# Kernel tuning notes

Measured on AMD Instinct MI355X. Metric: run time of the kernel, lower is better.

Reference implementation:

```python
import jax, jax.numpy as jnp
import numpy as np

D_MODEL = 1024
N_HEADS = 16
D_HEAD = D_MODEL // N_HEADS


def setup_inputs() -> dict:
    key = jax.random.key(0)
    k1, k2, k3 = jax.random.split(key, 3)
    x = jax.random.normal(k1, (4, 2048, D_MODEL), dtype=jnp.float32)
    # nn.Linear weights stored [out, in]; we keep that convention.
    s = 1.0 / np.sqrt(D_MODEL)
    W_qkv = jax.random.uniform(k2, (3 * D_MODEL, D_MODEL), dtype=jnp.float32, minval=-s, maxval=s)
    W_out = jax.random.uniform(k3, (D_MODEL, D_MODEL), dtype=jnp.float32, minval=-s, maxval=s)
    return {"x": x, "W_qkv": W_qkv, "W_out": W_out}


def reference(x, W_qkv, W_out):
    B, T, C = x.shape
    qkv = jnp.einsum('btc,oc->bto', x, W_qkv)  # [B,T,3C]
    q, k, v = jnp.split(qkv, 3, axis=-1)

    def split_heads(t):
        return t.reshape(B, T, N_HEADS, D_HEAD).transpose(0, 2, 1, 3)  # [B,H,T,Dh]

    q, k, v = split_heads(q), split_heads(k), split_heads(v)
    scale = D_HEAD ** -0.5
    scores = jnp.einsum('bhqd,bhkd->bhqk', q, k) * scale  # [B,H,T,T]
    mask = jnp.triu(jnp.ones((T, T), dtype=bool), k=1)
    scores = jnp.where(mask, -jnp.inf, scores)
    att = jax.nn.softmax(scores, axis=-1)
    out = jnp.einsum('bhqk,bhkd->bhqd', att, v)
    out = out.transpose(0, 2, 1, 3).reshape(B, T, C)
    return jnp.einsum('btc,oc->bto', out, W_out)
```

## Files before the change

### kernel.cpp

```cpp
#include <hip/hip_runtime.h>
#include <hip/hip_bf16.h>
#include <math.h>


typedef __attribute__((ext_vector_type(8))) short bf16x8;
typedef __attribute__((ext_vector_type(4))) float f32x4;

__device__ __forceinline__ void async16(const void* g, void* l) {
    __builtin_amdgcn_global_load_lds((const __attribute__((address_space(1))) void*)g,
                                     (__attribute__((address_space(3))) void*)l,
                                     16, 0, 0);
}

__device__ __forceinline__ unsigned short f2b(float f) {
    __hip_bfloat16 h = __float2bfloat16(f);
    return *(unsigned short*)&h;
}

__global__ __launch_bounds__(256)
void cast_f32_bf16(const float* __restrict__ in, unsigned short* __restrict__ out, int n)
{
    int i = (blockIdx.x * 256 + threadIdx.x) * 8;
    if (i + 8 > n) return;
    float4 a = *(const float4*)(in + i);
    float4 b = *(const float4*)(in + i + 4);
    __hip_bfloat16 r[8];
    r[0] = __float2bfloat16(a.x); r[1] = __float2bfloat16(a.y);
    r[2] = __float2bfloat16(a.z); r[3] = __float2bfloat16(a.w);
    r[4] = __float2bfloat16(b.x); r[5] = __float2bfloat16(b.y);
    r[6] = __float2bfloat16(b.z); r[7] = __float2bfloat16(b.w);
    *(float4*)(out + i) = *(float4*)r;
}

template <typename OutT>
__global__ __launch_bounds__(256)
void gemm_bf16_nt(const unsigned short* __restrict__ A,
                  const unsigned short* __restrict__ Bt,
                  OutT* __restrict__ C, int M, int N, int K,
                  int sc_ncols, float sc)
{
    __shared__ unsigned short As[128 * 32];
    __shared__ unsigned short Bs[128 * 32];
    const int tid  = threadIdx.x;
    const int lane = tid & 63;
    const int wave = tid >> 6;
    const int wm   = wave >> 1;
    const int wn   = wave & 1;
    const int m0   = blockIdx.y * 128;
    const int n0   = blockIdx.x * 128;

    f32x4 acc[4][4];
#pragma unroll
    for (int i = 0; i < 4; ++i)
#pragma unroll
        for (int j = 0; j < 4; ++j) acc[i][j] = (f32x4){0.f, 0.f, 0.f, 0.f};

    const int srow = tid >> 2;
    const int scol = (tid & 3) * 8;
    const int wbase = wave * 512;
    const int fr = lane & 15;
    const int fk = (lane >> 4) * 8;

    for (int k0 = 0; k0 < K; k0 += 32) {
#pragma unroll
        for (int c = 0; c < 2; ++c) {
            const unsigned short* ga = A + (size_t)(m0 + c * 64 + srow) * K + k0 + scol;
            async16(ga, As + c * 2048 + wbase);
            const unsigned short* gb = Bt + (size_t)(n0 + c * 64 + srow) * K + k0 + scol;
            async16(gb, Bs + c * 2048 + wbase);
        }
        __syncthreads();

        bf16x8 af[4], bfr[4];
#pragma unroll
        for (int mi = 0; mi < 4; ++mi)
            af[mi] = *(const bf16x8*)&As[(wm * 64 + mi * 16 + fr) * 32 + fk];
#pragma unroll
        for (int ni = 0; ni < 4; ++ni)
            bfr[ni] = *(const bf16x8*)&Bs[(wn * 64 + ni * 16 + fr) * 32 + fk];
#pragma unroll
        for (int mi = 0; mi < 4; ++mi)
#pragma unroll
            for (int ni = 0; ni < 4; ++ni)
                acc[mi][ni] = __builtin_amdgcn_mfma_f32_16x16x32_bf16(
                    af[mi], bfr[ni], acc[mi][ni], 0, 0, 0);
        __syncthreads();
    }

    const int ccol  = n0 + wn * 64 + (lane & 15);
    const int crow0 = m0 + wm * 64 + (lane >> 4) * 4;
#pragma unroll
    for (int mi = 0; mi < 4; ++mi) {
#pragma unroll
        for (int r = 0; r < 4; ++r) {
            const size_t row = (size_t)(crow0 + mi * 16 + r);
#pragma unroll
            for (int ni = 0; ni < 4; ++ni) {
                float mult = (ccol + ni * 16 < sc_ncols) ? sc : 1.0f;
                float v = acc[mi][ni][r] * mult;
                if constexpr (__is_same(OutT, float)) {
                    C[row * N + ccol + ni * 16] = v;
                } else {
                    C[row * N + ccol + ni * 16] = f2b(v);
                }
            }
        }
    }
}

__global__ __launch_bounds__(256)
void transpose_v(const unsigned short* __restrict__ qkv, unsigned short* __restrict__ vt, int T)
{
    __shared__ unsigned short tile[64 * 72];
    const int tid = threadIdx.x;
    const int k0  = blockIdx.x * 64;
    const int h   = blockIdx.y;
    const int b   = blockIdx.z;
    const size_t C3 = 3072;
    const unsigned short* vb = qkv + (size_t)b * T * C3 + 2048 + h * 64;

    const int r  = tid >> 2;
    const int c0 = (tid & 3) * 16;
    {
        const unsigned short* g = vb + (size_t)(k0 + r) * C3 + c0;
        *(float4*)&tile[r * 72 + c0]     = *(const float4*)g;
        *(float4*)&tile[r * 72 + c0 + 8] = *(const float4*)(g + 8);
    }
    __syncthreads();
    unsigned short buf[16];
#pragma unroll
    for (int j = 0; j < 16; ++j) buf[j] = tile[(c0 + j) * 72 + r];
    unsigned short* o = vt + ((size_t)(b * 16 + h) * 64 + r) * T + k0 + c0;
    *(float4*)o       = *(float4*)&buf[0];
    *(float4*)(o + 8) = *(float4*)&buf[8];
}

__global__ __launch_bounds__(256, 4)
void attn_mfma(const unsigned short* __restrict__ qkv,
               const unsigned short* __restrict__ vt,
               unsigned short* __restrict__ out, int T)
{
    __shared__ unsigned short Ks[64 * 72];
    __shared__ unsigned short Vts[64 * 72];
    __shared__ unsigned short Ps[64 * 72];

    const int tid  = threadIdx.x;
    const int lane = tid & 63;
    const int wave = tid >> 6;
    const int lc   = lane & 15;
    const int quad = lane >> 4;
    const int nq   = T >> 6;
    const int bid  = blockIdx.x;
    const int bh   = bid & 63;
    const int a    = bid >> 6;
    const int b    = bh >> 4;
    const int h    = bh & 15;
    int qt[2];
    qt[0] = nq - 1 - a;
    qt[1] = a;
    const size_t C3 = 3072;
    const unsigned short* qb  = qkv + (size_t)b * T * C3 + h * 64;
    const unsigned short* kb  = qb + 1024;
    const unsigned short* vtb = vt + (size_t)(b * 16 + h) * 64 * T;

    const int sr = tid >> 2;
    const int sc = (tid & 3) * 16;

    const int qrow = wave * 16 + lc;
    bf16x8 qf[2][2];
#pragma unroll
    for (int t = 0; t < 2; ++t) {
        const unsigned short* gq = qb + (size_t)(qt[t] * 64 + qrow) * C3 + quad * 8;
        qf[t][0] = *(const bf16x8*)gq;
        qf[t][1] = *(const bf16x8*)(gq + 32);
    }

    f32x4 o_[2][4];
    float l_[2][4];
#pragma unroll
    for (int t = 0; t < 2; ++t)
#pragma unroll
        for (int i = 0; i < 4; ++i) {
            o_[t][i] = (f32x4){0.f, 0.f, 0.f, 0.f};
            l_[t][i] = 0.f;
        }

    const float MB = 8.0f;

    for (int kt = 0; kt <= qt[0]; ++kt) {
        const int k0 = kt * 64;
        const unsigned short* gk = kb + (size_t)(k0 + sr) * C3 + sc;
        float4 kv0 = *(const float4*)gk;
        float4 kv1 = *(const float4*)(gk + 8);
        const unsigned short* gv = vtb + (size_t)sr * T + k0 + sc;
        float4 vv0 = *(const float4*)gv;
        float4 vv1 = *(const float4*)(gv + 8);

        __syncthreads();
        *(float4*)&Ks[sr * 72 + sc]      = kv0;
        *(float4*)&Ks[sr * 72 + sc + 8]  = kv1;
        *(float4*)&Vts[sr * 72 + sc]     = vv0;
        *(float4*)&Vts[sr * 72 + sc + 8] = vv1;
        __syncthreads();

#pragma unroll
        for (int t = 0; t < 2; ++t) {
            if (t == 1 && kt > qt[1]) break;
            const bool isdiag = (kt == qt[t]);

            f32x4 s[4];
#pragma unroll
            for (int ni = 0; ni < 4; ++ni) {
                bf16x8 bk0 = *(const bf16x8*)&Ks[(ni * 16 + lc) * 72 + quad * 8];
                bf16x8 bk1 = *(const bf16x8*)&Ks[(ni * 16 + lc) * 72 + 32 + quad * 8];
                s[ni] = (f32x4){0.f, 0.f, 0.f, 0.f};
                s[ni] = __builtin_amdgcn_mfma_f32_16x16x32_bf16(qf[t][0], bk0, s[ni], 0, 0, 0);
                s[ni] = __builtin_amdgcn_mfma_f32_16x16x32_bf16(qf[t][1], bk1, s[ni], 0, 0, 0);
            }
            if (isdiag) {
#pragma unroll
                for (int ni = 0; ni < 4; ++ni)
#pragma unroll
                    for (int r = 0; r < 4; ++r)
                        if (ni * 16 + lc > wave * 16 + quad * 4 + r)
                            s[ni][r] = -__builtin_inff();
            }
#pragma unroll
            for (int r = 0; r < 4; ++r) {
                float p0 = __builtin_amdgcn_exp2f(s[0][r] - MB);
                float p1 = __builtin_amdgcn_exp2f(s[1][r] - MB);
                float p2 = __builtin_amdgcn_exp2f(s[2][r] - MB);
                float p3 = __builtin_amdgcn_exp2f(s[3][r] - MB);
                l_[t][r] += (p0 + p1) + (p2 + p3);
                const int prow = (wave * 16 + quad * 4 + r) * 72;
                Ps[prow + lc]      = f2b(p0);
                Ps[prow + 16 + lc] = f2b(p1);
                Ps[prow + 32 + lc] = f2b(p2);
                Ps[prow + 48 + lc] = f2b(p3);
            }
            bf16x8 ap0 = *(const bf16x8*)&Ps[(wave * 16 + lc) * 72 + quad * 8];
            bf16x8 ap1 = *(const bf16x8*)&Ps[(wave * 16 + lc) * 72 + 32 + quad * 8];
#pragma unroll
            for (int ni = 0; ni < 4; ++ni) {
                bf16x8 bv0 = *(const bf16x8*)&Vts[(ni * 16 + lc) * 72 + quad * 8];
                bf16x8 bv1 = *(const bf16x8*)&Vts[(ni * 16 + lc) * 72 + 32 + quad * 8];
                o_[t][ni] = __builtin_amdgcn_mfma_f32_16x16x32_bf16(ap0, bv0, o_[t][ni], 0, 0, 0);
                o_[t][ni] = __builtin_amdgcn_mfma_f32_16x16x32_bf16(ap1, bv1, o_[t][ni], 0, 0, 0);
            }
        }
    }

#pragma unroll
    for (int t = 0; t < 2; ++t) {
        unsigned short* ob = out + ((size_t)b * T + qt[t] * 64 + wave * 16 + quad * 4) * 1024
                           + h * 64 + lc;
#pragma unroll
        for (int r = 0; r < 4; ++r) {
            float rs = l_[t][r];
#pragma unroll
            for (int off = 1; off < 16; off <<= 1)
                rs += __shfl_xor(rs, off, 16);
            float inv = 1.f / rs;
#pragma unroll
            for (int ni = 0; ni < 4; ++ni)
                ob[(size_t)r * 1024 + ni * 16] = f2b(o_[t][ni][r] * inv);
        }
    }
}

extern "C" void kernel_launch(void* const* d_in, const int* in_sizes, int n_in,
                              void* d_out, int out_size, void* d_ws, size_t ws_size,
                              hipStream_t stream)
{
    const float* x     = (const float*)d_in[0];
    const float* W_qkv = (const float*)d_in[1];
    const float* W_out = (const float*)d_in[2];
    float* out = (float*)d_out;

    const int C = 1024;
    const int T = 2048;
    const int M = in_sizes[0] / C;
    const int B = M / T;
    const int n_x    = in_sizes[0];
    const int n_wqkv = in_sizes[1];
    const int n_wout = in_sizes[2];

    unsigned short* x_bf    = (unsigned short*)d_ws;
    unsigned short* wqkv_bf = x_bf    + n_x;
    unsigned short* wout_bf = wqkv_bf + n_wqkv;
    unsigned short* qkv_bf  = wout_bf + n_wout;
    unsigned short* vt_bf   = qkv_bf  + (size_t)M * 3 * C;
    unsigned short* ao_bf   = vt_bf   + (size_t)B * 16 * 64 * T;

    cast_f32_bf16<<<n_x    / 2048, 256, 0, stream>>>(x,     x_bf,    n_x);
    cast_f32_bf16<<<n_wqkv / 2048, 256, 0, stream>>>(W_qkv, wqkv_bf, n_wqkv);
    cast_f32_bf16<<<n_wout / 2048, 256, 0, stream>>>(W_out, wout_bf, n_wout);

    const float QSC = 0.18033688011112042f;
    gemm_bf16_nt<unsigned short><<<dim3((3*C)/128, M/128), 256, 0, stream>>>(
        x_bf, wqkv_bf, qkv_bf, M, 3*C, C, C, QSC);

    transpose_v<<<dim3(T/64, 16, B), 256, 0, stream>>>(qkv_bf, vt_bf, T);

    const int nq = T / 64;
    attn_mfma<<<dim3(B * 16 * (nq / 2)), 256, 0, stream>>>(qkv_bf, vt_bf, ao_bf, T);

    gemm_bf16_nt<float><<<dim3(C/128, M/128), 256, 0, stream>>>(
        ao_bf, wout_bf, out, M, C, C, 0, 1.0f);
}
```

Baseline: 272.9 us.

## Transpose attention MFMA operands so scores land per-query-row in lanes

Swaps MFMA operand order (K and V^T as A, Q and P as B) so each lane holds four consecutive key/feature values for one query row. This allows packed bf16x2 stores of P to LDS and of the output to global memory, and a per-lane row-sum reduced with two shuffles instead of four shuffle rounds per row. K and V fragments are hoisted out of the per-tile loop and shared by both query tiles, and P gets a double buffer so both tiles' softmax can run before either PV matmul. The cost is higher register pressure from the hoisted fragments under launch_bounds(256,4), plus extra LDS for the second P buffer.

```diff
diff --git a/kernel.cpp b/kernel.cpp
--- a/kernel.cpp
+++ b/kernel.cpp
@@ -15,6 +15,11 @@
 __device__ __forceinline__ unsigned short f2b(float f) {
     __hip_bfloat16 h = __float2bfloat16(f);
     return *(unsigned short*)&h;
+}
+
+__device__ __forceinline__ unsigned int packbf2(float a, float b) {
+    __hip_bfloat162 h2 = __float22bfloat162_rn(make_float2(a, b));
+    return *(unsigned int*)&h2;
 }
 
 __global__ __launch_bounds__(256)
@@ -142,7 +147,7 @@
 {
     __shared__ unsigned short Ks[64 * 72];
     __shared__ unsigned short Vts[64 * 72];
-    __shared__ unsigned short Ps[64 * 72];
+    __shared__ unsigned short Ps[2][64 * 72];
 
     const int tid  = threadIdx.x;
     const int lane = tid & 63;
@@ -176,14 +181,13 @@
     }
 
     f32x4 o_[2][4];
-    float l_[2][4];
-#pragma unroll
-    for (int t = 0; t < 2; ++t)
-#pragma unroll
-        for (int i = 0; i < 4; ++i) {
-            o_[t][i] = (f32x4){0.f, 0.f, 0.f, 0.f};
-            l_[t][i] = 0.f;
-        }
+    float l_[2];
+#pragma unroll
+    for (int t = 0; t < 2; ++t) {
+        l_[t] = 0.f;
+#pragma unroll
+        for (int i = 0; i < 4; ++i) o_[t][i] = (f32x4){0.f, 0.f, 0.f, 0.f};
+    }
 
     const float MB = 8.0f;
 
@@ -203,67 +207,84 @@
         *(float4*)&Vts[sr * 72 + sc + 8] = vv1;
         __syncthreads();
 
+        bf16x8 ak[4][2];
+#pragma unroll
+        for (int mi = 0; mi < 4; ++mi) {
+            ak[mi][0] = *(const bf16x8*)&Ks[(mi * 16 + lc) * 72 + quad * 8];
+            ak[mi][1] = *(const bf16x8*)&Ks[(mi * 16 + lc) * 72 + 32 + quad * 8];
+        }
+
 #pragma unroll
         for (int t = 0; t < 2; ++t) {
             if (t == 1 && kt > qt[1]) break;
-            const bool isdiag = (kt == qt[t]);
-
             f32x4 s[4];
 #pragma unroll
-            for (int ni = 0; ni < 4; ++ni) {
-                bf16x8 bk0 = *(const bf16x8*)&Ks[(ni * 16 + lc) * 72 + quad * 8];
-                bf16x8 bk1 = *(const bf16x8*)&Ks[(ni * 16 + lc) * 72 + 32 + quad * 8];
-                s[ni] = (f32x4){0.f, 0.f, 0.f, 0.f};
-                s[ni] = __builtin_amdgcn_mfma_f32_16x16x32_bf16(qf[t][0], bk0, s[ni], 0, 0, 0);
-                s[ni] = __builtin_amdgcn_mfma_f32_16x16x32_bf16(qf[t][1], bk1, s[ni], 0, 0, 0);
-            }
-            if (isdiag) {
-#pragma unroll
-                for (int ni = 0; ni < 4; ++ni)
+            for (int mi = 0; mi < 4; ++mi) {
+                s[mi] = (f32x4){0.f, 0.f, 0.f, 0.f};
+                s[mi] = __builtin_amdgcn_mfma_f32_16x16x32_bf16(ak[mi][0], qf[t][0], s[mi], 0, 0, 0);
+                s[mi] = __builtin_amdgcn_mfma_f32_16x16x32_bf16(ak[mi][1], qf[t][1], s[mi], 0, 0, 0);
+            }
+            if (kt == qt[t]) {
+                const int qg = qt[t] * 64 + wave * 16 + lc;
+                const int kbase = k0 + quad * 4;
+#pragma unroll
+                for (int mi = 0; mi < 4; ++mi)
 #pragma unroll
                     for (int r = 0; r < 4; ++r)
-                        if (ni * 16 + lc > wave * 16 + quad * 4 + r)
-                            s[ni][r] = -__builtin_inff();
-            }
-#pragma unroll
-            for (int r = 0; r < 4; ++r) {
-                float p0 = __builtin_amdgcn_exp2f(s[0][r] - MB);
-                float p1 = __builtin_amdgcn_exp2f(s[1][r] - MB);
-                float p2 = __builtin_amdgcn_exp2f(s[2][r] - MB);
-                float p3 = __builtin_amdgcn_exp2f(s[3][r] - MB);
-                l_[t][r] += (p0 + p1) + (p2 + p3);
-                const int prow = (wave * 16 + quad * 4 + r) * 72;
-                Ps[prow + lc]      = f2b(p0);
-                Ps[prow + 16 + lc] = f2b(p1);
-                Ps[prow + 32 + lc] = f2b(p2);
-                Ps[prow + 48 + lc] = f2b(p3);
-            }
-            bf16x8 ap0 = *(const bf16x8*)&Ps[(wave * 16 + lc) * 72 + quad * 8];
-            bf16x8 ap1 = *(const bf16x8*)&Ps[(wave * 16 + lc) * 72 + 32 + quad * 8];
-#pragma unroll
-            for (int ni = 0; ni < 4; ++ni) {
-                bf16x8 bv0 = *(const bf16x8*)&Vts[(ni * 16 + lc) * 72 + quad * 8];
-                bf16x8 bv1 = *(const bf16x8*)&Vts[(ni * 16 + lc) * 72 + 32 + quad * 8];
-                o_[t][ni] = __builtin_amdgcn_mfma_f32_16x16x32_bf16(ap0, bv0, o_[t][ni], 0, 0, 0);
-                o_[t][ni] = __builtin_amdgcn_mfma_f32_16x16x32_bf16(ap1, bv1, o_[t][ni], 0, 0, 0);
+                        if (kbase + mi * 16 + r > qg)
+                            s[mi][r] = -__builtin_inff();
+            }
+            float lacc = 0.f;
+            const int prow = (wave * 16 + lc) * 72 + quad * 4;
+#pragma unroll
+            for (int mi = 0; mi < 4; ++mi) {
+                float p0 = __builtin_amdgcn_exp2f(s[mi][0] - MB);
+                float p1 = __builtin_amdgcn_exp2f(s[mi][1] - MB);
+                float p2 = __builtin_amdgcn_exp2f(s[mi][2] - MB);
+                float p3 = __builtin_amdgcn_exp2f(s[mi][3] - MB);
+                lacc += (p0 + p1) + (p2 + p3);
+                uint2 pk;
+                pk.x = packbf2(p0, p1);
+                pk.y = packbf2(p2, p3);
+                *(uint2*)&Ps[t][prow + mi * 16] = pk;
+            }
+            l_[t] += lacc;
+        }
+
+        bf16x8 av[4][2];
+#pragma unroll
+        for (int mi = 0; mi < 4; ++mi) {
+            av[mi][0] = *(const bf16x8*)&Vts[(mi * 16 + lc) * 72 + quad * 8];
+            av[mi][1] = *(const bf16x8*)&Vts[(mi * 16 + lc) * 72 + 32 + quad * 8];
+        }
+
+#pragma unroll
+        for (int t = 0; t < 2; ++t) {
+            if (t == 1 && kt > qt[1]) break;
+            bf16x8 bp0 = *(const bf16x8*)&Ps[t][(wave * 16 + lc) * 72 + quad * 8];
+            bf16x8 bp1 = *(const bf16x8*)&Ps[t][(wave * 16 + lc) * 72 + 32 + quad * 8];
+#pragma unroll
+            for (int mi = 0; mi < 4; ++mi) {
+                o_[t][mi] = __builtin_amdgcn_mfma_f32_16x16x32_bf16(av[mi][0], bp0, o_[t][mi], 0, 0, 0);
+                o_[t][mi] = __builtin_amdgcn_mfma_f32_16x16x32_bf16(av[mi][1], bp1, o_[t][mi], 0, 0, 0);
             }
         }
     }
 
 #pragma unroll
     for (int t = 0; t < 2; ++t) {
-        unsigned short* ob = out + ((size_t)b * T + qt[t] * 64 + wave * 16 + quad * 4) * 1024
-                           + h * 64 + lc;
-#pragma unroll
-        for (int r = 0; r < 4; ++r) {
-            float rs = l_[t][r];
-#pragma unroll
-            for (int off = 1; off < 16; off <<= 1)
-                rs += __shfl_xor(rs, off, 16);
-            float inv = 1.f / rs;
-#pragma unroll
-            for (int ni = 0; ni < 4; ++ni)
-                ob[(size_t)r * 1024 + ni * 16] = f2b(o_[t][ni][r] * inv);
+        float rs = l_[t];
+        rs += __shfl_xor(rs, 16);
+        rs += __shfl_xor(rs, 32);
+        float inv = 1.f / rs;
+        unsigned short* ob = out + ((size_t)b * T + qt[t] * 64 + wave * 16 + lc) * 1024
+                           + h * 64 + quad * 4;
+#pragma unroll
+        for (int mi = 0; mi < 4; ++mi) {
+            uint2 pk;
+            pk.x = packbf2(o_[t][mi][0] * inv, o_[t][mi][1] * inv);
+            pk.y = packbf2(o_[t][mi][2] * inv, o_[t][mi][3] * inv);
+            *(uint2*)(ob + mi * 16) = pk;
         }
     }
 }
```

After: 263.9 us. -3.3%, faster.
